# Performance work log

Hardware: AMD Instinct MI355X
Metric: run time of the kernel (lower is better)

Reference implementation:

```python
import jax, jax.numpy as jnp
import numpy as np

NUM_HEADS = 12
HIDDEN = 768
HEAD_DIM = HIDDEN // NUM_HEADS  # 64
B, S = 2, 2048


def setup_inputs() -> dict:
    key = jax.random.key(0)
    ks = jax.random.split(key, 8)
    inp = {
        "hidden_states": jax.random.normal(ks[0], (B, S, HIDDEN), dtype=jnp.float32),
        "attention_mask": jnp.zeros((B, 1, 1, S), dtype=jnp.float32),
        "Wq": jax.random.normal(ks[1], (HIDDEN, HIDDEN), dtype=jnp.float32) * 0.02,
        "bq": jnp.zeros((HIDDEN,), dtype=jnp.float32),
        "Wk": jax.random.normal(ks[2], (HIDDEN, HIDDEN), dtype=jnp.float32) * 0.02,
        "bk": jnp.zeros((HIDDEN,), dtype=jnp.float32),
        "Wv": jax.random.normal(ks[3], (HIDDEN, HIDDEN), dtype=jnp.float32) * 0.02,
        "bv": jnp.zeros((HIDDEN,), dtype=jnp.float32),
    }
    return inp


def _split_heads(x):
    # [B, S, H*d] -> [B, H, S, d]
    b, s, _ = x.shape
    return x.reshape(b, s, NUM_HEADS, HEAD_DIM).transpose(0, 2, 1, 3)


def reference(hidden_states, attention_mask, Wq, bq, Wk, bk, Wv, bv):
    # Q/K/V projections (nn.Linear: x @ W.T + b; W generated square so direct matmul is equivalent math)
    q = _split_heads(hidden_states @ Wq + bq)  # [B,H,S,d]
    k = _split_heads(hidden_states @ Wk + bk)
    v = _split_heads(hidden_states @ Wv + bv)

    scale = 1.0 / np.sqrt(HEAD_DIM).astype(np.float32)
    scores = jnp.einsum("bhqd,bhkd->bhqk", q, k) * scale  # [B,H,S,S]
    scores = scores + attention_mask  # additive mask, broadcast [B,1,1,S]
    probs = jax.nn.softmax(scores, axis=-1)
    # dropout prob = 0.0 -> identity (eval mode)
    ctx = jnp.einsum("bhqk,bhkd->bhqd", probs, v)  # [B,H,S,d]
    ctx = ctx.transpose(0, 2, 1, 3).reshape(hidden_states.shape[0], hidden_states.shape[1], HIDDEN)
    return ctx
```

## Files before the change

kernel.cpp:

```cpp
#include <hip/hip_runtime.h>

#define S_LEN 2048
#define HID   768
#define NH    12
#define HD    64
#define BATCH 2
#define GK    768
#define L2E   1.44269504088896340736f
#define QSCL  (0.125f * L2E)

typedef __attribute__((ext_vector_type(8))) short bf16x8;
typedef __attribute__((ext_vector_type(4))) float f32x4;
typedef __attribute__((ext_vector_type(4))) short s16x4;
typedef __attribute__((ext_vector_type(8))) short s16x8;

__device__ __forceinline__ unsigned short f2bf(float f) {
    union { float f; unsigned int u; } v; v.f = f;
    unsigned int r = v.u + 0x7fffu + ((v.u >> 16) & 1u);
    return (unsigned short)(r >> 16);
}
__device__ __forceinline__ unsigned short f2bf_hu(float f) {
    union { float f; unsigned int u; } v; v.f = f;
    return (unsigned short)((v.u + 0x8000u) >> 16);
}

__device__ __forceinline__ unsigned int cvtpk(float a, float b) {
    unsigned int r;
    asm("v_cvt_pk_bf16_f32 %0, %1, %2" : "=v"(r) : "v"(a), "v"(b));
    return r;
}

#if __has_builtin(__builtin_amdgcn_exp2f)
#define EXP2(x) __builtin_amdgcn_exp2f(x)
#else
__device__ __forceinline__ float EXP2(float x) {
    float r;
    asm volatile("v_exp_f32 %0, %1\n\ts_nop 0" : "=v"(r) : "v"(x));
    return r;
}
#endif

#define GLL16(gp, lp) __builtin_amdgcn_global_load_lds( \
    (const __attribute__((address_space(1))) unsigned int*)(gp), \
    (__attribute__((address_space(3))) unsigned int*)(lp), 16, 0, 0)


__global__ __launch_bounds__(256) void prep_kernel(
    const float* __restrict__ X, const float* __restrict__ Wq,
    const float* __restrict__ Wk, const float* __restrict__ Wv,
    const float* __restrict__ maskg,
    unsigned short* __restrict__ Xb, unsigned short* __restrict__ Wt,
    float* __restrict__ wsm) {
    __shared__ float T[32][33];
    int bid = blockIdx.x;
    if (bid >= 4800) {
        int idx = (bid - 4800) * 256 + threadIdx.x;
        float4 v = ((const float4*)maskg)[idx];
        float4 s; s.x = v.x*L2E; s.y = v.y*L2E; s.z = v.z*L2E; s.w = v.w*L2E;
        ((float4*)wsm)[idx] = s;
        return;
    }
    if (bid < 3072) {
        int id = bid * 256 + threadIdx.x;
        float4 v = ((const float4*)X)[id];
        s16x4 o; o[0] = (short)f2bf(v.x); o[1] = (short)f2bf(v.y);
        o[2] = (short)f2bf(v.z); o[3] = (short)f2bf(v.w);
        ((s16x4*)Xb)[id] = o;
        return;
    }
    int t2 = bid - 3072;
    int mat = t2 / 576, t = t2 % 576;
    int tk = t / 24, tn = t % 24;
    const float* W = (mat == 0) ? Wq : (mat == 1) ? Wk : Wv;
    const float scl = (mat == 0) ? QSCL : 1.0f;
    int r  = threadIdx.x >> 3;
    int c4 = (threadIdx.x & 7) * 4;
    float4 v = *(const float4*)&W[(size_t)(tk*32 + r) * GK + tn*32 + c4];
    T[c4+0][r] = v.x; T[c4+1][r] = v.y; T[c4+2][r] = v.z; T[c4+3][r] = v.w;
    __syncthreads();
    s16x4 o;
    o[0] = (short)f2bf(T[r][c4+0] * scl); o[1] = (short)f2bf(T[r][c4+1] * scl);
    o[2] = (short)f2bf(T[r][c4+2] * scl); o[3] = (short)f2bf(T[r][c4+3] * scl);
    *(s16x4*)&Wt[(size_t)(mat*768 + tn*32 + r) * GK + tk*32 + c4] = o;
}

__global__ __launch_bounds__(256) void gemm_qkv(
    const unsigned short* __restrict__ Xb, const unsigned short* __restrict__ Wt,
    const float* __restrict__ bq, const float* __restrict__ bk,
    const float* __restrict__ bv,
    unsigned short* __restrict__ qb, unsigned short* __restrict__ kb,
    unsigned short* __restrict__ vb) {
    __shared__ __align__(16) unsigned short As[128][64];
    __shared__ __align__(16) unsigned short Bs[128][64];

    const int tid = threadIdx.x;
    const int wgid = blockIdx.y * gridDim.x + blockIdx.x;
    const int virt = (wgid & 7) * 72 + (wgid >> 3);
    const int bm = (virt / 18) * 128;
    const int bn = (virt % 18) * 128;
    const int w = tid >> 6, l = tid & 63, quad = l >> 4, lq = l & 15;
    const int wx = w & 1, wy = w >> 1;

    const int srow = l >> 3, schunk = ((l & 7) ^ (l >> 3)) * 8;
    const unsigned short* aga = Xb + (size_t)(bm + w*32 + srow) * GK + schunk;
    const unsigned short* bga = Wt + (size_t)(bn + w*32 + srow) * GK + schunk;

    const int c0 = ((quad)     ^ (lq & 7)) * 8;
    const int c1 = ((4 + quad) ^ (lq & 7)) * 8;

    f32x4 zero = {0.f, 0.f, 0.f, 0.f};
    f32x4 acc[4][4];
#pragma unroll
    for (int mi = 0; mi < 4; mi++)
#pragma unroll
        for (int ni = 0; ni < 4; ni++) acc[mi][ni] = zero;

    for (int k0 = 0; k0 < GK; k0 += 64) {
        __syncthreads();
#pragma unroll
        for (int i = 0; i < 4; i++) {
            GLL16(aga + k0 + i*8*GK, &As[w*32 + i*8][0]);
            GLL16(bga + k0 + i*8*GK, &Bs[w*32 + i*8][0]);
        }
        __syncthreads();
#pragma unroll
        for (int kh = 0; kh < 2; kh++) {
            const int cc = kh ? c1 : c0;
            bf16x8 a[4], b[4];
#pragma unroll
            for (int mi = 0; mi < 4; mi++)
                a[mi] = *(const bf16x8*)&As[wy*64 + mi*16 + lq][cc];
#pragma unroll
            for (int ni = 0; ni < 4; ni++)
                b[ni] = *(const bf16x8*)&Bs[wx*64 + ni*16 + lq][cc];
#pragma unroll
            for (int mi = 0; mi < 4; mi++)
#pragma unroll
                for (int ni = 0; ni < 4; ni++)
                    acc[mi][ni] = __builtin_amdgcn_mfma_f32_16x16x32_bf16(
                        a[mi], b[ni], acc[mi][ni], 0, 0, 0);
        }
    }

    const int mat = bn / 768;
    const float* bias = (mat == 0) ? bq : (mat == 1) ? bk : bv;
    const float bscl = (mat == 0) ? QSCL : 1.0f;
    const int nbase = bn % 768;
#pragma unroll
    for (int ni = 0; ni < 4; ni++) {
        int hn = nbase + wx*64 + ni*16 + lq;
        float bval = bias[hn] * bscl;
        int h = hn >> 6, d = hn & 63;
#pragma unroll
        for (int mi = 0; mi < 4; mi++) {
            int m0 = bm + wy*64 + mi*16 + quad*4;
            int b_ = m0 >> 11, s0 = m0 & 2047;
            if (mat != 1) {
                unsigned short* outp = (mat == 0) ? qb : vb;
                s16x4 pk;
#pragma unroll
                for (int r = 0; r < 4; r++) pk[r] = (short)f2bf_hu(acc[mi][ni][r] + bval);
                *(s16x4*)&outp[((size_t)((b_*NH + h) * HD + d)) * S_LEN + s0] = pk;
            } else {
                size_t base = ((size_t)((b_*NH + h) * S_LEN + s0)) * HD + d;
#pragma unroll
                for (int r = 0; r < 4; r++)
                    kb[base + (size_t)r * HD] = f2bf_hu(acc[mi][ni][r] + bval);
            }
        }
    }
}

__global__ __launch_bounds__(256, 4) void attn_kernel(
    const unsigned short* __restrict__ Qtg, const unsigned short* __restrict__ Kg,
    const unsigned short* __restrict__ Vtg, const float* __restrict__ wsm,
    float* __restrict__ out) {
    __shared__ __align__(16) unsigned short Ks[2][64][64];
    __shared__ __align__(16) unsigned short Vt[2][64][64];
    __shared__ __align__(16) unsigned short Ps[4][16][64];

    const int tid = threadIdx.x;
    const int w = tid >> 6, l = tid & 63, quad = l >> 4, lq = l & 15;

    const int wgid = blockIdx.y * gridDim.x + blockIdx.x;
    const int virt = (wgid & 7) * 96 + (wgid >> 3);
    const int bh = virt >> 5;
    const int q0 = (virt & 31) * 64;
    const int bi = bh / NH, hi = bh % NH;
    const unsigned short* Kh = Kg + (size_t)bh * S_LEN * HD;
    const unsigned short* Vh = Vtg + (size_t)bh * HD * S_LEN;
    const float* wsmb = wsm + (size_t)bi * S_LEN;

    bf16x8 a0, a1;
    {
        const unsigned short* Qt = Qtg + (size_t)bh * HD * S_LEN + (q0 + w*16 + lq);
#pragma unroll
        for (int j = 0; j < 8; j++) {
            a0[j] = (short)Qt[(size_t)(quad*8 + j) * S_LEN];
            a1[j] = (short)Qt[(size_t)(quad*8 + j + 32) * S_LEN];
        }
    }

    bf16x8 ones;
#pragma unroll
    for (int i = 0; i < 8; i++) ones[i] = (short)0x3F80;

    const int srow = l >> 3, schunk = ((l & 7) ^ (l >> 3)) * 8;
    const unsigned short* kga = Kh + (size_t)(w*16 + srow) * HD + schunk;
    const unsigned short* vga = Vh + (size_t)(w*16 + srow) * S_LEN + schunk;

    const int c0 = ((quad)     ^ (lq & 7)) * 8;
    const int c1 = ((4 + quad) ^ (lq & 7)) * 8;
    const int pqh = quad >> 1;
    const int po  = (quad & 1) * 4;
    const int pe  = lq & 7;

    f32x4 zero = {0.f, 0.f, 0.f, 0.f};
    f32x4 o[4], lsum = zero;
#pragma unroll
    for (int ng = 0; ng < 4; ng++) o[ng] = zero;

    auto stage = [&](int buf, int kt) {
#pragma unroll
        for (int i = 0; i < 2; i++) {
            GLL16(kga + (size_t)kt*64*HD + i*8*HD, &Ks[buf][w*16 + i*8][0]);
            GLL16(vga + kt*64 + (size_t)i*8*S_LEN, &Vt[buf][w*16 + i*8][0]);
        }
    };

    auto ldm = [&](f32x4* dst, int kt) {
#pragma unroll
        for (int g = 0; g < 4; g++)
            dst[g] = *(const f32x4*)&wsmb[kt*64 + g*16 + quad*4];
    };

    auto compute = [&](int buf, const f32x4* mk) {
        f32x4 st[4];
#pragma unroll
        for (int g = 0; g < 4; g++) {
            bf16x8 b0 = *(const bf16x8*)&Ks[buf][g*16 + lq][c0];
            bf16x8 b1 = *(const bf16x8*)&Ks[buf][g*16 + lq][c1];
            f32x4 z = __builtin_amdgcn_mfma_f32_16x16x32_bf16(b0, a0, mk[g], 0, 0, 0);
            st[g]   = __builtin_amdgcn_mfma_f32_16x16x32_bf16(b1, a1, z,     0, 0, 0);
        }

#pragma unroll
        for (int g = 0; g < 4; g++) {
            float p0 = EXP2(st[g][0]);
            float p1 = EXP2(st[g][1]);
            float p2 = EXP2(st[g][2]);
            float p3 = EXP2(st[g][3]);
            uint2 pr;
            pr.x = cvtpk(p0, p1);
            pr.y = cvtpk(p2, p3);
            *(uint2*)&Ps[w][lq][((g*2 + pqh) ^ pe) * 8 + po] = pr;
        }

        bf16x8 pa0 = *(const bf16x8*)&Ps[w][lq][c0];
        bf16x8 pa1 = *(const bf16x8*)&Ps[w][lq][c1];

        lsum = __builtin_amdgcn_mfma_f32_16x16x32_bf16(pa0, ones, lsum, 0, 0, 0);
        lsum = __builtin_amdgcn_mfma_f32_16x16x32_bf16(pa1, ones, lsum, 0, 0, 0);

#pragma unroll
        for (int ng = 0; ng < 4; ng++) {
            bf16x8 v0 = *(const bf16x8*)&Vt[buf][ng*16 + lq][c0];
            bf16x8 v1 = *(const bf16x8*)&Vt[buf][ng*16 + lq][c1];
            f32x4 t = __builtin_amdgcn_mfma_f32_16x16x32_bf16(pa0, v0, o[ng], 0, 0, 0);
            o[ng]   = __builtin_amdgcn_mfma_f32_16x16x32_bf16(pa1, v1, t,     0, 0, 0);
        }
    };

    f32x4 mkA[4], mkB[4];
    ldm(mkA, 0);
    stage(0, 0);
    __syncthreads();

    for (int kt = 0; kt < S_LEN / 64; kt += 2) {
        stage(1, kt + 1); ldm(mkB, kt + 1);
        compute(0, mkA);
        __syncthreads();
        if (kt + 2 < S_LEN / 64) { stage(0, kt + 2); ldm(mkA, kt + 2); }
        compute(1, mkB);
        __syncthreads();
    }

#pragma unroll
    for (int r = 0; r < 4; r++) {
        const float inv = 1.0f / lsum[r];
        const int row = q0 + w*16 + quad*4 + r;
#pragma unroll
        for (int ng = 0; ng < 4; ng++)
            out[((size_t)(bi * S_LEN + row)) * HID + hi*HD + ng*16 + lq] = o[ng][r] * inv;
    }
}

extern "C" void kernel_launch(void* const* d_in, const int* in_sizes, int n_in,
                              void* d_out, int out_size, void* d_ws, size_t ws_size,
                              hipStream_t stream) {
    const float* X    = (const float*)d_in[0];
    const float* mask = (const float*)d_in[1];
    const float* Wq   = (const float*)d_in[2];
    const float* bq   = (const float*)d_in[3];
    const float* Wk   = (const float*)d_in[4];
    const float* bk   = (const float*)d_in[5];
    const float* Wv   = (const float*)d_in[6];
    const float* bv   = (const float*)d_in[7];
    float* out = (float*)d_out;

    const size_t per = (size_t)BATCH * NH * S_LEN * HD;
    unsigned short* qb = (unsigned short*)d_ws;
    unsigned short* kb = qb + per;
    unsigned short* vb = kb + per;
    unsigned short* xb = vb + per;
    unsigned short* wt = xb + (size_t)4096 * GK;
    float* wsm = (float*)(wt + (size_t)2304 * GK);

    prep_kernel<<<4804, 256, 0, stream>>>(X, Wq, Wk, Wv, mask, xb, wt, wsm);

    dim3 ggrid(18, 32);
    gemm_qkv<<<ggrid, 256, 0, stream>>>(xb, wt, bq, bk, bv, qb, kb, vb);

    dim3 agrid(S_LEN / 64, BATCH * NH);
    attn_kernel<<<agrid, 256, 0, stream>>>(qb, kb, vb, wsm, out);
}
```

Before: 155.7 us.

## Keep attention probabilities in registers via permuted K rows; halve GEMM N-tile

The attention kernel now permutes which K rows each lane reads, and adjusts the mask load to match, so that the exp'd score accumulators already sit in the MFMA A-operand layout for P·V. This removes the per-tile LDS round trip through the Ps buffer. The K staging swizzle changes to fit the new access pattern. Separately, the QKV GEMM tile shrinks from 128x128 to 128x64, doubling the grid to 1152 blocks for better CU occupancy at the cost of less operand reuse per block.

```diff
diff --git a/kernel.cpp b/kernel.cpp
--- a/kernel.cpp
+++ b/kernel.cpp
@@ -43,7 +43,6 @@
 #define GLL16(gp, lp) __builtin_amdgcn_global_load_lds( \
     (const __attribute__((address_space(1))) unsigned int*)(gp), \
     (__attribute__((address_space(3))) unsigned int*)(lp), 16, 0, 0)
-
 
 __global__ __launch_bounds__(256) void prep_kernel(
     const float* __restrict__ X, const float* __restrict__ Wq,
@@ -91,52 +90,53 @@
     unsigned short* __restrict__ qb, unsigned short* __restrict__ kb,
     unsigned short* __restrict__ vb) {
     __shared__ __align__(16) unsigned short As[128][64];
-    __shared__ __align__(16) unsigned short Bs[128][64];
+    __shared__ __align__(16) unsigned short Bs[64][64];
 
     const int tid = threadIdx.x;
     const int wgid = blockIdx.y * gridDim.x + blockIdx.x;
-    const int virt = (wgid & 7) * 72 + (wgid >> 3);
-    const int bm = (virt / 18) * 128;
-    const int bn = (virt % 18) * 128;
+    const int virt = (wgid & 7) * 144 + (wgid >> 3);
+    const int bm = (virt / 36) * 128;
+    const int bn = (virt % 36) * 64;
     const int w = tid >> 6, l = tid & 63, quad = l >> 4, lq = l & 15;
     const int wx = w & 1, wy = w >> 1;
 
     const int srow = l >> 3, schunk = ((l & 7) ^ (l >> 3)) * 8;
     const unsigned short* aga = Xb + (size_t)(bm + w*32 + srow) * GK + schunk;
-    const unsigned short* bga = Wt + (size_t)(bn + w*32 + srow) * GK + schunk;
+    const unsigned short* bga = Wt + (size_t)(bn + w*16 + srow) * GK + schunk;
 
     const int c0 = ((quad)     ^ (lq & 7)) * 8;
     const int c1 = ((4 + quad) ^ (lq & 7)) * 8;
 
     f32x4 zero = {0.f, 0.f, 0.f, 0.f};
-    f32x4 acc[4][4];
+    f32x4 acc[4][2];
 #pragma unroll
     for (int mi = 0; mi < 4; mi++)
 #pragma unroll
-        for (int ni = 0; ni < 4; ni++) acc[mi][ni] = zero;
+        for (int ni = 0; ni < 2; ni++) acc[mi][ni] = zero;
 
     for (int k0 = 0; k0 < GK; k0 += 64) {
         __syncthreads();
 #pragma unroll
-        for (int i = 0; i < 4; i++) {
+        for (int i = 0; i < 4; i++)
             GLL16(aga + k0 + i*8*GK, &As[w*32 + i*8][0]);
-            GLL16(bga + k0 + i*8*GK, &Bs[w*32 + i*8][0]);
-        }
+#pragma unroll
+        for (int i = 0; i < 2; i++)
+            GLL16(bga + k0 + i*8*GK, &Bs[w*16 + i*8][0]);
         __syncthreads();
 #pragma unroll
         for (int kh = 0; kh < 2; kh++) {
             const int cc = kh ? c1 : c0;
-            bf16x8 a[4], b[4];
+            bf16x8 a[4], b[2];
 #pragma unroll
             for (int mi = 0; mi < 4; mi++)
                 a[mi] = *(const bf16x8*)&As[wy*64 + mi*16 + lq][cc];
 #pragma unroll
-            for (int ni = 0; ni < 4; ni++)
-                b[ni] = *(const bf16x8*)&Bs[wx*64 + ni*16 + lq][cc];
+            for (int ni = 0; ni < 2; ni++)
+                b[ni] = *(const bf16x8*)&Bs[wx*32 + ni*16 + lq][cc];
 #pragma unroll
             for (int mi = 0; mi < 4; mi++)
 #pragma unroll
-                for (int ni = 0; ni < 4; ni++)
+                for (int ni = 0; ni < 2; ni++)
                     acc[mi][ni] = __builtin_amdgcn_mfma_f32_16x16x32_bf16(
                         a[mi], b[ni], acc[mi][ni], 0, 0, 0);
         }
@@ -147,8 +147,8 @@
     const float bscl = (mat == 0) ? QSCL : 1.0f;
     const int nbase = bn % 768;
 #pragma unroll
-    for (int ni = 0; ni < 4; ni++) {
-        int hn = nbase + wx*64 + ni*16 + lq;
+    for (int ni = 0; ni < 2; ni++) {
+        int hn = nbase + wx*32 + ni*16 + lq;
         float bval = bias[hn] * bscl;
         int h = hn >> 6, d = hn & 63;
 #pragma unroll
@@ -177,7 +177,6 @@
     float* __restrict__ out) {
     __shared__ __align__(16) unsigned short Ks[2][64][64];
     __shared__ __align__(16) unsigned short Vt[2][64][64];
-    __shared__ __align__(16) unsigned short Ps[4][16][64];
 
     const int tid = threadIdx.x;
     const int w = tid >> 6, l = tid & 63, quad = l >> 4, lq = l & 15;
@@ -205,15 +204,19 @@
 #pragma unroll
     for (int i = 0; i < 8; i++) ones[i] = (short)0x3F80;
 
-    const int srow = l >> 3, schunk = ((l & 7) ^ (l >> 3)) * 8;
-    const unsigned short* kga = Kh + (size_t)(w*16 + srow) * HD + schunk;
-    const unsigned short* vga = Vh + (size_t)(w*16 + srow) * S_LEN + schunk;
+    const int srow = l >> 3;
+    const int svchunk = ((l & 7) ^ (l >> 3)) * 8;
+    const unsigned short* vga = Vh + (size_t)(w*16 + srow) * S_LEN + svchunk;
+    const int ckK = ((l & 7) ^ ((l >> 3) & 3)) * 8;
+    const unsigned short* kga0 = Kh + (size_t)(w*16 + srow) * HD + ckK;
+    const unsigned short* kga1 = Kh + (size_t)(w*16 + 8 + srow) * HD + (ckK ^ 32);
 
     const int c0 = ((quad)     ^ (lq & 7)) * 8;
     const int c1 = ((4 + quad) ^ (lq & 7)) * 8;
-    const int pqh = quad >> 1;
-    const int po  = (quad & 1) * 4;
-    const int pe  = lq & 7;
+    const int fk  = (lq & 3) | (((lq >> 2) & 1) << 2);
+    const int kc0 = (quad ^ fk) * 8;
+    const int kc1 = kc0 ^ 32;
+    const int krA = (lq >> 2) * 8 + (lq & 3);
 
     f32x4 zero = {0.f, 0.f, 0.f, 0.f};
     f32x4 o[4], lsum = zero;
@@ -221,43 +224,47 @@
     for (int ng = 0; ng < 4; ng++) o[ng] = zero;
 
     auto stage = [&](int buf, int kt) {
-#pragma unroll
-        for (int i = 0; i < 2; i++) {
-            GLL16(kga + (size_t)kt*64*HD + i*8*HD, &Ks[buf][w*16 + i*8][0]);
-            GLL16(vga + kt*64 + (size_t)i*8*S_LEN, &Vt[buf][w*16 + i*8][0]);
-        }
+        GLL16(kga0 + (size_t)kt*64*HD, &Ks[buf][w*16][0]);
+        GLL16(kga1 + (size_t)kt*64*HD, &Ks[buf][w*16 + 8][0]);
+        GLL16(vga + kt*64,                   &Vt[buf][w*16][0]);
+        GLL16(vga + kt*64 + (size_t)8*S_LEN, &Vt[buf][w*16 + 8][0]);
     };
 
     auto ldm = [&](f32x4* dst, int kt) {
-#pragma unroll
-        for (int g = 0; g < 4; g++)
-            dst[g] = *(const f32x4*)&wsmb[kt*64 + g*16 + quad*4];
+        const float* mb = wsmb + kt*64 + quad*8;
+        dst[0] = *(const f32x4*)(mb);
+        dst[1] = *(const f32x4*)(mb + 4);
+        dst[2] = *(const f32x4*)(mb + 32);
+        dst[3] = *(const f32x4*)(mb + 36);
     };
 
     auto compute = [&](int buf, const f32x4* mk) {
         f32x4 st[4];
 #pragma unroll
-        for (int g = 0; g < 4; g++) {
-            bf16x8 b0 = *(const bf16x8*)&Ks[buf][g*16 + lq][c0];
-            bf16x8 b1 = *(const bf16x8*)&Ks[buf][g*16 + lq][c1];
-            f32x4 z = __builtin_amdgcn_mfma_f32_16x16x32_bf16(b0, a0, mk[g], 0, 0, 0);
-            st[g]   = __builtin_amdgcn_mfma_f32_16x16x32_bf16(b1, a1, z,     0, 0, 0);
-        }
-
-#pragma unroll
-        for (int g = 0; g < 4; g++) {
-            float p0 = EXP2(st[g][0]);
-            float p1 = EXP2(st[g][1]);
-            float p2 = EXP2(st[g][2]);
-            float p3 = EXP2(st[g][3]);
-            uint2 pr;
-            pr.x = cvtpk(p0, p1);
-            pr.y = cvtpk(p2, p3);
-            *(uint2*)&Ps[w][lq][((g*2 + pqh) ^ pe) * 8 + po] = pr;
-        }
-
-        bf16x8 pa0 = *(const bf16x8*)&Ps[w][lq][c0];
-        bf16x8 pa1 = *(const bf16x8*)&Ps[w][lq][c1];
+        for (int c = 0; c < 4; c++) {
+            const int roff = (c & 1) * 4 + (c >> 1) * 32;
+            bf16x8 b0 = *(const bf16x8*)&Ks[buf][krA + roff][kc0];
+            bf16x8 b1 = *(const bf16x8*)&Ks[buf][krA + roff][kc1];
+            f32x4 z = __builtin_amdgcn_mfma_f32_16x16x32_bf16(b0, a0, mk[c], 0, 0, 0);
+            st[c]   = __builtin_amdgcn_mfma_f32_16x16x32_bf16(b1, a1, z,     0, 0, 0);
+        }
+
+        union PU { unsigned int d[4]; bf16x8 v; } p0u, p1u;
+#pragma unroll
+        for (int c = 0; c < 2; c++) {
+            float e0 = EXP2(st[c][0]), e1 = EXP2(st[c][1]);
+            float e2 = EXP2(st[c][2]), e3 = EXP2(st[c][3]);
+            p0u.d[c*2]   = cvtpk(e0, e1);
+            p0u.d[c*2+1] = cvtpk(e2, e3);
+        }
+#pragma unroll
+        for (int c = 0; c < 2; c++) {
+            float e0 = EXP2(st[2+c][0]), e1 = EXP2(st[2+c][1]);
+            float e2 = EXP2(st[2+c][2]), e3 = EXP2(st[2+c][3]);
+            p1u.d[c*2]   = cvtpk(e0, e1);
+            p1u.d[c*2+1] = cvtpk(e2, e3);
+        }
+        bf16x8 pa0 = p0u.v, pa1 = p1u.v;
 
         lsum = __builtin_amdgcn_mfma_f32_16x16x32_bf16(pa0, ones, lsum, 0, 0, 0);
         lsum = __builtin_amdgcn_mfma_f32_16x16x32_bf16(pa1, ones, lsum, 0, 0, 0);
@@ -318,7 +325,7 @@
 
     prep_kernel<<<4804, 256, 0, stream>>>(X, Wq, Wk, Wv, mask, xb, wt, wsm);
 
-    dim3 ggrid(18, 32);
+    dim3 ggrid(36, 32);
     gemm_qkv<<<ggrid, 256, 0, stream>>>(xb, wt, bq, bk, bv, qb, kb, vb);
 
     dim3 agrid(S_LEN / 64, BATCH * NH);
```

After: 147.4 us (median of 2 runs). 5.4% less time.
